# Performance work log

Measured on AMD Instinct MI355X. Metric: run time of the kernel, lower is better.

Reference implementation:

```python
import jax, jax.numpy as jnp
import numpy as np

B, S, H, NH = 8, 1024, 1024, 16
HD = H // NH  # 64


def _rope(x, cos, sin):
    # x: [B, NH, S, HD]; cos/sin: [1, 1, S, HD]
    x1, x2 = jnp.split(x, 2, axis=-1)
    x_rot = jnp.concatenate((-x2, x1), axis=-1)
    return x * cos + x_rot * sin


def setup_inputs() -> dict:
    key = jax.random.key(0)
    ks = jax.random.split(key, 12)
    std = 1.0 / np.sqrt(H)
    inp = {
        "hidden_states": jax.random.normal(ks[0], (B, S, H), dtype=jnp.float32),
        "cos": jax.random.uniform(ks[1], (S, HD), dtype=jnp.float32),
        "sin": jax.random.uniform(ks[2], (S, HD), dtype=jnp.float32),
        "Wq": jax.random.normal(ks[3], (H, H), dtype=jnp.float32) * std,
        "bq": jnp.zeros((H,), dtype=jnp.float32),
        "Wk": jax.random.normal(ks[4], (H, H), dtype=jnp.float32) * std,
        "bk": jnp.zeros((H,), dtype=jnp.float32),
        "Wv": jax.random.normal(ks[5], (H, H), dtype=jnp.float32) * std,
        "bv": jnp.zeros((H,), dtype=jnp.float32),
        "Wo": jax.random.normal(ks[6], (H, H), dtype=jnp.float32) * std,
        "bo": jnp.zeros((H,), dtype=jnp.float32),
    }
    return inp


def reference(hidden_states, cos, sin, Wq, bq, Wk, bk, Wv, bv, Wo, bo):
    def split_heads(t):  # [B,S,H] -> [B,NH,S,HD]
        return t.reshape(B, S, NH, HD).transpose(0, 2, 1, 3)

    q = split_heads(hidden_states @ Wq.T + bq)
    k = split_heads(hidden_states @ Wk.T + bk)
    v = split_heads(hidden_states @ Wv.T + bv)

    c = cos.reshape(1, 1, S, HD)
    s = sin.reshape(1, 1, S, HD)
    q = _rope(q, c, s)
    k = _rope(k, c, s)

    scale = 1.0 / jnp.sqrt(jnp.asarray(HD, dtype=q.dtype))
    scores = jnp.einsum("bhqd,bhkd->bhqk", q, k) * scale
    attn = jax.nn.softmax(scores, axis=-1)
    out = jnp.einsum("bhqk,bhkd->bhqd", attn, v)  # [B,NH,S,HD]
    out = out.transpose(0, 2, 1, 3).reshape(B, S, H)
    return out @ Wo.T + bo
```

## Files before the change

### kernel.cpp

```cpp
#include <hip/hip_runtime.h>
#include <hip/hip_bf16.h>
#include <stdint.h>


typedef __bf16 bf16_t;
typedef __bf16 bf16x8 __attribute__((ext_vector_type(8)));
typedef __bf16 bf16x4 __attribute__((ext_vector_type(4)));
typedef float  f32x4  __attribute__((ext_vector_type(4)));
typedef uint32_t u32x4 __attribute__((ext_vector_type(4)));

typedef __attribute__((address_space(1))) const void* as1_cvp;
typedef __attribute__((address_space(3))) void* as3_vp;

__device__ __forceinline__ f32x4 mfma16(bf16x8 a, bf16x8 b, f32x4 c) {
  return __builtin_amdgcn_mfma_f32_16x16x32_bf16(a, b, c, 0, 0, 0);
}

__device__ __forceinline__ void gload_lds16(const bf16_t* g, bf16_t* l) {
  __builtin_amdgcn_global_load_lds((as1_cvp)g, (as3_vp)l, 16, 0, 0);
}

__device__ __forceinline__ f32x4 zero4() {
  f32x4 z = {0.f, 0.f, 0.f, 0.f};
  return z;
}

__global__ void cvt_all(const float* __restrict__ hs, const float* __restrict__ wq,
                        const float* __restrict__ wk, const float* __restrict__ wv,
                        const float* __restrict__ wo, bf16_t* __restrict__ Xb,
                        bf16_t* __restrict__ Wqkvb, bf16_t* __restrict__ Wob) {
  const int i = blockIdx.x * 256 + threadIdx.x;
  const f32x4* src;
  bf16x4* dst;
  if (i < 2097152) {
    src = (const f32x4*)hs + i;            dst = (bf16x4*)Xb + i;
  } else if (i < 2359296) {
    src = (const f32x4*)wq + (i - 2097152); dst = (bf16x4*)Wqkvb + (i - 2097152);
  } else if (i < 2621440) {
    src = (const f32x4*)wk + (i - 2359296); dst = (bf16x4*)Wqkvb + (i - 2359296) + 262144;
  } else if (i < 2883584) {
    src = (const f32x4*)wv + (i - 2621440); dst = (bf16x4*)Wqkvb + (i - 2621440) + 524288;
  } else {
    src = (const f32x4*)wo + (i - 2883584); dst = (bf16x4*)Wob + (i - 2883584);
  }
  const f32x4 v = *src;
  bf16x4 o;
  o[0] = (bf16_t)v[0]; o[1] = (bf16_t)v[1];
  o[2] = (bf16_t)v[2]; o[3] = (bf16_t)v[3];
  *dst = o;
}

template <int MODE>
__global__ __launch_bounds__(256, 3) void gemm128(
    const bf16_t* __restrict__ A, const bf16_t* __restrict__ Bw,
    const float* __restrict__ bQ, const float* __restrict__ bK,
    const float* __restrict__ bV, const float* __restrict__ cosp,
    const float* __restrict__ sinp,
    bf16_t* __restrict__ Qb, bf16_t* __restrict__ Kb, bf16_t* __restrict__ Vtb,
    float* __restrict__ Cout) {
  __shared__ bf16_t sm[128 * 64 * 2];
  bf16_t* sA = sm;
  bf16_t* sB = sm + 128 * 64;

  const int tid = threadIdx.x;
  const int lane = tid & 63;
  const int wid = tid >> 6;
  const int l15 = lane & 15;
  const int l4 = lane >> 4;
  const int row0 = blockIdx.x * 128;
  const int col0 = blockIdx.y * 128;
  const int wr = (wid >> 1) * 64;
  const int wc = (wid & 1) * 64;

  f32x4 acc[4][4];
#pragma unroll
  for (int mi = 0; mi < 4; ++mi)
#pragma unroll
    for (int ni = 0; ni < 4; ++ni) acc[mi][ni] = zero4();

  for (int kt = 0; kt < 16; ++kt) {
    const int k0 = kt * 64;
#pragma unroll
    for (int i = 0; i < 4; ++i) {
      const int chunk = i * 256 + tid;
      const int r = chunk >> 3, cc = chunk & 7;
      const int scc = cc ^ (r & 7);
      gload_lds16(A + (size_t)(row0 + r) * 1024 + k0 + scc * 8,
                  sA + (i * 256 + wid * 64) * 8);
      gload_lds16(Bw + (size_t)(col0 + r) * 1024 + k0 + scc * 8,
                  sB + (i * 256 + wid * 64) * 8);
    }
    __syncthreads();
    __builtin_amdgcn_s_setprio(1);
#pragma unroll
    for (int ks = 0; ks < 2; ++ks) {
      bf16x8 af[4], bfv[4];
#pragma unroll
      for (int mi = 0; mi < 4; ++mi) {
        const int r = wr + mi * 16 + l15;
        af[mi] = *(const bf16x8*)(sA + r * 64 + (((ks * 4 + l4) ^ (r & 7)) << 3));
      }
#pragma unroll
      for (int ni = 0; ni < 4; ++ni) {
        const int r = wc + ni * 16 + l15;
        bfv[ni] = *(const bf16x8*)(sB + r * 64 + (((ks * 4 + l4) ^ (r & 7)) << 3));
      }
#pragma unroll
      for (int mi = 0; mi < 4; ++mi)
#pragma unroll
        for (int ni = 0; ni < 4; ++ni)
          acc[mi][ni] = mfma16(af[mi], bfv[ni], acc[mi][ni]);
    }
    __builtin_amdgcn_s_setprio(0);
    __syncthreads();
  }

  if constexpr (MODE == 0) {
    const int proj = blockIdx.y >> 3;
    const float* bias = proj == 0 ? bQ : (proj == 1 ? bK : bV);
    if (proj < 2) {
      bf16_t* dst = proj == 0 ? Qb : Kb;
      const float qs = proj == 0 ? 0.18033688011112042f : 1.0f;
      const int base = col0 & 1023;
#pragma unroll
      for (int mi = 0; mi < 4; ++mi)
#pragma unroll
        for (int nl = 0; nl < 2; ++nl) {
          const int gcL = base + wc + nl * 16 + l15;
          const int h = gcL >> 6, dL = gcL & 63;
          const float bbL = bias[gcL], bbH = bias[gcL + 32];
#pragma unroll
          for (int j = 0; j < 4; ++j) {
            const int gr = row0 + wr + mi * 16 + l4 * 4 + j;
            const int b = gr >> 10, s = gr & 1023;
            const float cL = cosp[s * 64 + dL], cH = cosp[s * 64 + dL + 32];
            const float snL = sinp[s * 64 + dL], snH = sinp[s * 64 + dL + 32];
            const float x1 = acc[mi][nl][j] + bbL;
            const float x2 = acc[mi][nl + 2][j] + bbH;
            bf16_t* p = dst + ((size_t)(b * 16 + h) * 1024 + s) * 64 + dL;
            p[0]  = (bf16_t)((x1 * cL - x2 * snL) * qs);
            p[32] = (bf16_t)((x2 * cH + x1 * snH) * qs);
          }
        }
    } else {
      bf16_t* trb = sm;
#pragma unroll
      for (int mi = 0; mi < 4; ++mi)
#pragma unroll
        for (int ni = 0; ni < 4; ++ni) {
          const int cl = wc + ni * 16 + l15;
          const float bb = bias[(col0 & 1023) + cl];
#pragma unroll
          for (int j = 0; j < 4; ++j) {
            const int rl = wr + mi * 16 + l4 * 4 + j;
            trb[cl * 128 + (((rl >> 3) ^ (cl & 7)) << 3) + (rl & 7)] =
                (bf16_t)(acc[mi][ni][j] + bb);
          }
        }
      __syncthreads();
      const int b = row0 >> 10, s0 = row0 & 1023;
#pragma unroll
      for (int i = 0; i < 8; ++i) {
        const int chunk = i * 256 + tid;
        const int cl = chunk >> 4, rc = chunk & 15;
        const u32x4 v = *(const u32x4*)(trb + cl * 128 + ((rc ^ (cl & 7)) << 3));
        const int cv = (col0 & 1023) + cl;
        *(u32x4*)(Vtb + ((size_t)(b * 16 + (cv >> 6)) * 64 + (cv & 63)) * 1024 +
                  s0 + rc * 8) = v;
      }
    }
  } else {
#pragma unroll
    for (int mi = 0; mi < 4; ++mi)
#pragma unroll
      for (int ni = 0; ni < 4; ++ni) {
        const int gc = col0 + wc + ni * 16 + l15;
        const float bb = bQ[gc];
#pragma unroll
        for (int j = 0; j < 4; ++j) {
          const int gr = row0 + wr + mi * 16 + l4 * 4 + j;
          Cout[(size_t)gr * 1024 + gc] = acc[mi][ni][j] + bb;
        }
      }
  }
}

__global__ __launch_bounds__(256, 4) void attn_kernel(
    const bf16_t* __restrict__ Qb, const bf16_t* __restrict__ Kb,
    const bf16_t* __restrict__ Vtb, bf16_t* __restrict__ AOb) {
  __shared__ bf16_t sm[16384];
  bf16_t* sK = sm;
  bf16_t* sV = sm + 4096;
  const int tid = threadIdx.x, lane = tid & 63, wid = tid >> 6;
  const int l15 = lane & 15, l4 = lane >> 4;
  bf16_t* sP = sm + 8192 + wid * 2048;

  const int bh = blockIdx.x;
  const int q0 = blockIdx.y * 128;
  const bf16_t* Qg = Qb + (size_t)bh * 65536;
  const bf16_t* Kg = Kb + (size_t)bh * 65536;
  const bf16_t* Vg = Vtb + (size_t)bh * 65536;

#pragma unroll
  for (int i = 0; i < 4; ++i) {
    const int chunk = i * 256 + tid, r = chunk >> 3, c = chunk & 7;
    *(u32x4*)(sm + r * 64 + ((c ^ (r & 7)) << 3)) =
        *(const u32x4*)(Qg + (size_t)(q0 + r) * 64 + c * 8);
  }
  __syncthreads();
  bf16x8 qf[2][2];
#pragma unroll
  for (int mi = 0; mi < 2; ++mi)
#pragma unroll
    for (int kq = 0; kq < 2; ++kq) {
      const int r = wid * 32 + mi * 16 + l15;
      qf[mi][kq] =
          *(const bf16x8*)(sm + r * 64 + (((kq * 4 + l4) ^ (r & 7)) << 3));
    }
  __syncthreads();

  const int ck0 = tid, ck1 = 256 + tid;
  const int kr0 = ck0 >> 3, kc0 = ck0 & 7;
  const int kr1 = ck1 >> 3, kc1 = ck1 & 7;
  bf16_t* kd0 = sK + kr0 * 64 + ((kc0 ^ (kr0 & 7)) << 3);
  bf16_t* kd1 = sK + kr1 * 64 + ((kc1 ^ (kr1 & 7)) << 3);
  bf16_t* vd0 = sV + kr0 * 64 + ((kc0 ^ (kr0 & 7)) << 3);
  bf16_t* vd1 = sV + kr1 * 64 + ((kc1 ^ (kr1 & 7)) << 3);
  const bf16_t* ksrc0 = Kg + kr0 * 64 + kc0 * 8;
  const bf16_t* ksrc1 = Kg + kr1 * 64 + kc1 * 8;
  const bf16_t* vsrc0 = Vg + kr0 * 1024 + kc0 * 8;
  const bf16_t* vsrc1 = Vg + kr1 * 1024 + kc1 * 8;

  u32x4 kv0 = *(const u32x4*)ksrc0;
  u32x4 kv1 = *(const u32x4*)ksrc1;
  u32x4 kv2 = *(const u32x4*)vsrc0;
  u32x4 kv3 = *(const u32x4*)vsrc1;

  f32x4 oacc[2][4];
  float l_p[2] = {0.f, 0.f};
#pragma unroll
  for (int mi = 0; mi < 2; ++mi)
#pragma unroll
    for (int no = 0; no < 4; ++no) oacc[mi][no] = zero4();

  for (int kt = 0; kt < 16; ++kt) {
    *(u32x4*)kd0 = kv0;
    *(u32x4*)kd1 = kv1;
    *(u32x4*)vd0 = kv2;
    *(u32x4*)vd1 = kv3;
    __syncthreads();
    if (kt < 15) {
      kv0 = *(const u32x4*)(ksrc0 + (kt + 1) * 4096);
      kv1 = *(const u32x4*)(ksrc1 + (kt + 1) * 4096);
      kv2 = *(const u32x4*)(vsrc0 + (kt + 1) * 64);
      kv3 = *(const u32x4*)(vsrc1 + (kt + 1) * 64);
    }

    f32x4 st[2][4];
    __builtin_amdgcn_s_setprio(1);
#pragma unroll
    for (int ni = 0; ni < 4; ++ni) {
      const int r = ni * 16 + l15;
      const bf16x8 kf0 = *(const bf16x8*)(sK + r * 64 + ((l4 ^ (r & 7)) << 3));
      const bf16x8 kf1 =
          *(const bf16x8*)(sK + r * 64 + (((4 + l4) ^ (r & 7)) << 3));
      st[0][ni] = mfma16(kf1, qf[0][1], mfma16(kf0, qf[0][0], zero4()));
      st[1][ni] = mfma16(kf1, qf[1][1], mfma16(kf0, qf[1][0], zero4()));
    }
    __builtin_amdgcn_s_setprio(0);

#pragma unroll
    for (int mi = 0; mi < 2; ++mi) {
      float rs = 0.f;
      const int rl = mi * 16 + l15;
#pragma unroll
      for (int ni = 0; ni < 4; ++ni) {
        bf16x4 pk;
#pragma unroll
        for (int j = 0; j < 4; ++j) {
          const float p = __builtin_amdgcn_exp2f(st[mi][ni][j]);
          rs += p;
          pk[j] = (bf16_t)p;
        }
        const int chunk = (ni * 2 + (l4 >> 1)) ^ (rl & 7);
        *(bf16x4*)(sP + rl * 64 + (chunk << 3) + ((l4 & 1) << 2)) = pk;
      }
      l_p[mi] += rs;
    }

    __builtin_amdgcn_s_setprio(1);
#pragma unroll
    for (int ks = 0; ks < 2; ++ks) {
      bf16x8 pa[2];
#pragma unroll
      for (int mi = 0; mi < 2; ++mi) {
        const int rl = mi * 16 + l15;
        pa[mi] =
            *(const bf16x8*)(sP + rl * 64 + (((ks * 4 + l4) ^ (rl & 7)) << 3));
      }
#pragma unroll
      for (int no = 0; no < 4; ++no) {
        const int hd = no * 16 + l15;
        const bf16x8 vf =
            *(const bf16x8*)(sV + hd * 64 + (((ks * 4 + l4) ^ (hd & 7)) << 3));
        oacc[0][no] = mfma16(pa[0], vf, oacc[0][no]);
        oacc[1][no] = mfma16(pa[1], vf, oacc[1][no]);
      }
    }
    __builtin_amdgcn_s_setprio(0);
    __syncthreads();
  }

  float l_f[2];
#pragma unroll
  for (int mi = 0; mi < 2; ++mi) {
    float t = l_p[mi];
    t += __shfl_xor(t, 16);
    t += __shfl_xor(t, 32);
    l_f[mi] = t;
  }

  const int b = bh >> 4, h = bh & 15;
#pragma unroll
  for (int mi = 0; mi < 2; ++mi)
#pragma unroll
    for (int j = 0; j < 4; ++j) {
      const float li = __builtin_amdgcn_rcpf(__shfl(l_f[mi], l4 * 4 + j));
      const int s = q0 + wid * 32 + mi * 16 + l4 * 4 + j;
#pragma unroll
      for (int no = 0; no < 4; ++no) {
        const int d = no * 16 + l15;
        AOb[((size_t)b * 1024 + s) * 1024 + h * 64 + d] =
            (bf16_t)(oacc[mi][no][j] * li);
      }
    }
}

extern "C" void kernel_launch(void* const* d_in, const int* in_sizes, int n_in,
                              void* d_out, int out_size, void* d_ws,
                              size_t ws_size, hipStream_t stream) {
  const float* hs = (const float*)d_in[0];
  const float* cs = (const float*)d_in[1];
  const float* sn = (const float*)d_in[2];
  const float* Wq = (const float*)d_in[3];
  const float* bq = (const float*)d_in[4];
  const float* Wk = (const float*)d_in[5];
  const float* bk = (const float*)d_in[6];
  const float* Wv = (const float*)d_in[7];
  const float* bv = (const float*)d_in[8];
  const float* Wo = (const float*)d_in[9];
  const float* bo = (const float*)d_in[10];
  float* out = (float*)d_out;

  char* ws = (char*)d_ws;
  bf16_t* Xb    = (bf16_t*)(ws + 0);
  bf16_t* Wqkvb = (bf16_t*)(ws + 16777216);
  bf16_t* Wob   = (bf16_t*)(ws + 23068672);
  bf16_t* Qb    = (bf16_t*)(ws + 25165824);
  bf16_t* Kb    = (bf16_t*)(ws + 41943040);
  bf16_t* Vtb   = (bf16_t*)(ws + 58720256);
  bf16_t* AOb   = (bf16_t*)(ws + 75497472);

  cvt_all<<<12288, 256, 0, stream>>>(hs, Wq, Wk, Wv, Wo, Xb, Wqkvb, Wob);
  gemm128<0><<<dim3(64, 24), 256, 0, stream>>>(Xb, Wqkvb, bq, bk, bv, cs, sn,
                                               Qb, Kb, Vtb, nullptr);
  attn_kernel<<<dim3(128, 8), 256, 0, stream>>>(Qb, Kb, Vtb, AOb);
  gemm128<1><<<dim3(64, 8), 256, 0, stream>>>(AOb, Wob, bo, nullptr, nullptr,
                                              nullptr, nullptr, nullptr,
                                              nullptr, nullptr, out);
}
```

Before: 138.2 us.

## Use 256x256 double-buffered 8-wave GEMM with interleaved prefetch for QKV projection

Replaces the 128x128 QKV projection GEMM with a 256x256-tile, 512-thread kernel. It double-buffers 128 KB of dynamic LDS and issues direct global-to-LDS prefetches of the next K tile between MFMA phases. The split into four sub-phases with barriers and priority bumps is meant to overlap memory traffic with compute and raise data reuse per tile. In exchange the grid drops to 384 blocks, occupancy falls, and the V transpose epilogue now needs two passes.

```diff
diff --git a/kernel.cpp b/kernel.cpp
--- a/kernel.cpp
+++ b/kernel.cpp
@@ -50,18 +50,200 @@
   *dst = o;
 }
 
-template <int MODE>
-__global__ __launch_bounds__(256, 3) void gemm128(
+__global__ __launch_bounds__(512, 2) void gemm256_qkv(
     const bf16_t* __restrict__ A, const bf16_t* __restrict__ Bw,
     const float* __restrict__ bQ, const float* __restrict__ bK,
     const float* __restrict__ bV, const float* __restrict__ cosp,
     const float* __restrict__ sinp,
-    bf16_t* __restrict__ Qb, bf16_t* __restrict__ Kb, bf16_t* __restrict__ Vtb,
-    float* __restrict__ Cout) {
+    bf16_t* __restrict__ Qb, bf16_t* __restrict__ Kb, bf16_t* __restrict__ Vtb) {
+  extern __shared__ bf16_t smem[];
+  const int tid = threadIdx.x;
+  const int lane = tid & 63, wid = tid >> 6;
+  const int l15 = lane & 15, l4 = lane >> 4;
+  const int wr = wid >> 2, wc = wid & 3;
+  const int row0 = blockIdx.x * 256, col0 = blockIdx.y * 256;
+
+  const int rr = tid >> 3, cc8 = tid & 7;
+  const int sc = cc8 ^ (rr & 7);
+  const bf16_t* pAs = A + (size_t)(row0 + rr) * 1024 + sc * 8;
+  const bf16_t* pBs = Bw + (size_t)(col0 + rr) * 1024 + sc * 8;
+  const int dA = wid * 512;
+
+  f32x4 acc[8][4];
+#pragma unroll
+  for (int mi = 0; mi < 8; ++mi)
+#pragma unroll
+    for (int ni = 0; ni < 4; ++ni) acc[mi][ni] = zero4();
+
+#pragma unroll
+  for (int k = 0; k < 4; ++k)
+    gload_lds16(pAs + (size_t)k * 65536, smem + k * 4096 + dA);
+#pragma unroll
+  for (int k = 0; k < 4; ++k)
+    gload_lds16(pBs + (size_t)k * 65536, smem + 16384 + k * 4096 + dA);
+  asm volatile("s_waitcnt vmcnt(0)" ::: "memory");
+  __builtin_amdgcn_s_barrier();
+
+#pragma unroll 2
+  for (int t = 0; t < 16; ++t) {
+    const int cur = t & 1;
+    bf16_t* sA = smem + cur * 32768;
+    bf16_t* sB = sA + 16384;
+    bf16_t* oD = smem + (cur ^ 1) * 32768;
+    const size_t ko = (size_t)(t + 1) * 64;
+
+    bf16x8 a0[4][2], a1[4][2], b0[2][2], b1[2][2];
+#pragma unroll
+    for (int mi = 0; mi < 4; ++mi) {
+      const int r = wr * 128 + mi * 16 + l15;
+#pragma unroll
+      for (int ks = 0; ks < 2; ++ks)
+        a0[mi][ks] = *(const bf16x8*)(sA + r * 64 + (((ks * 4 + l4) ^ (r & 7)) << 3));
+    }
+#pragma unroll
+    for (int n = 0; n < 2; ++n) {
+      const int r = wc * 64 + n * 16 + l15;
+#pragma unroll
+      for (int ks = 0; ks < 2; ++ks)
+        b0[n][ks] = *(const bf16x8*)(sB + r * 64 + (((ks * 4 + l4) ^ (r & 7)) << 3));
+    }
+    if (t < 15) {
+#pragma unroll
+      for (int k = 0; k < 4; ++k)
+        gload_lds16(pAs + (size_t)k * 65536 + ko, oD + k * 4096 + dA);
+    }
+    __builtin_amdgcn_s_barrier();
+    __builtin_amdgcn_s_setprio(1);
+#pragma unroll
+    for (int mi = 0; mi < 4; ++mi)
+#pragma unroll
+      for (int n = 0; n < 2; ++n)
+        acc[mi][n] = mfma16(a0[mi][1], b0[n][1],
+                            mfma16(a0[mi][0], b0[n][0], acc[mi][n]));
+    __builtin_amdgcn_s_setprio(0);
+    __builtin_amdgcn_s_barrier();
+
+#pragma unroll
+    for (int mi = 0; mi < 4; ++mi) {
+      const int r = wr * 128 + (mi + 4) * 16 + l15;
+#pragma unroll
+      for (int ks = 0; ks < 2; ++ks)
+        a1[mi][ks] = *(const bf16x8*)(sA + r * 64 + (((ks * 4 + l4) ^ (r & 7)) << 3));
+    }
+    if (t < 15) {
+#pragma unroll
+      for (int k = 0; k < 4; ++k)
+        gload_lds16(pBs + (size_t)k * 65536 + ko, oD + 16384 + k * 4096 + dA);
+    }
+    __builtin_amdgcn_s_barrier();
+    __builtin_amdgcn_s_setprio(1);
+#pragma unroll
+    for (int mi = 0; mi < 4; ++mi)
+#pragma unroll
+      for (int n = 0; n < 2; ++n)
+        acc[mi + 4][n] = mfma16(a1[mi][1], b0[n][1],
+                                mfma16(a1[mi][0], b0[n][0], acc[mi + 4][n]));
+    __builtin_amdgcn_s_setprio(0);
+    __builtin_amdgcn_s_barrier();
+
+#pragma unroll
+    for (int n = 0; n < 2; ++n) {
+      const int r = wc * 64 + (n + 2) * 16 + l15;
+#pragma unroll
+      for (int ks = 0; ks < 2; ++ks)
+        b1[n][ks] = *(const bf16x8*)(sB + r * 64 + (((ks * 4 + l4) ^ (r & 7)) << 3));
+    }
+    __builtin_amdgcn_s_barrier();
+    __builtin_amdgcn_s_setprio(1);
+#pragma unroll
+    for (int mi = 0; mi < 4; ++mi)
+#pragma unroll
+      for (int n = 0; n < 2; ++n)
+        acc[mi][n + 2] = mfma16(a0[mi][1], b1[n][1],
+                                mfma16(a0[mi][0], b1[n][0], acc[mi][n + 2]));
+    __builtin_amdgcn_s_setprio(0);
+    __builtin_amdgcn_s_barrier();
+
+    __builtin_amdgcn_s_setprio(1);
+#pragma unroll
+    for (int mi = 0; mi < 4; ++mi)
+#pragma unroll
+      for (int n = 0; n < 2; ++n)
+        acc[mi + 4][n + 2] = mfma16(a1[mi][1], b1[n][1],
+                                    mfma16(a1[mi][0], b1[n][0], acc[mi + 4][n + 2]));
+    __builtin_amdgcn_s_setprio(0);
+    if (t < 15) asm volatile("s_waitcnt vmcnt(0)" ::: "memory");
+    __builtin_amdgcn_s_barrier();
+  }
+
+  const int proj = col0 >> 10;
+  const int colp = col0 & 1023;
+  if (proj < 2) {
+    const float* bias = proj == 0 ? bQ : bK;
+    bf16_t* dst = proj == 0 ? Qb : Kb;
+    const float qs = proj == 0 ? 0.18033688011112042f : 1.0f;
+#pragma unroll
+    for (int mi = 0; mi < 8; ++mi)
+#pragma unroll
+      for (int nl = 0; nl < 2; ++nl) {
+        const int gcL = colp + wc * 64 + nl * 16 + l15;
+        const int h = gcL >> 6, dL = gcL & 63;
+        const float bbL = bias[gcL], bbH = bias[gcL + 32];
+#pragma unroll
+        for (int j = 0; j < 4; ++j) {
+          const int gr = row0 + wr * 128 + mi * 16 + l4 * 4 + j;
+          const int b = gr >> 10, s = gr & 1023;
+          const float cL = cosp[s * 64 + dL], cH = cosp[s * 64 + dL + 32];
+          const float snL = sinp[s * 64 + dL], snH = sinp[s * 64 + dL + 32];
+          const float x1 = acc[mi][nl][j] + bbL;
+          const float x2 = acc[mi][nl + 2][j] + bbH;
+          bf16_t* p = dst + ((size_t)(b * 16 + h) * 1024 + s) * 64 + dL;
+          p[0]  = (bf16_t)((x1 * cL - x2 * snL) * qs);
+          p[32] = (bf16_t)((x2 * cH + x1 * snH) * qs);
+        }
+      }
+  } else {
+    const int b = row0 >> 10, s0 = row0 & 1023;
+    __syncthreads();
+    bf16_t* trb = smem;
+#pragma unroll
+    for (int pass = 0; pass < 2; ++pass) {
+      if (wr == pass) {
+#pragma unroll
+        for (int mi = 0; mi < 8; ++mi)
+#pragma unroll
+          for (int ni = 0; ni < 4; ++ni) {
+            const int cl = wc * 64 + ni * 16 + l15;
+            const float bb = bV[colp + cl];
+#pragma unroll
+            for (int j = 0; j < 4; ++j) {
+              const int rl = mi * 16 + l4 * 4 + j;
+              trb[cl * 128 + (((rl >> 3) ^ (cl & 7)) << 3) + (rl & 7)] =
+                  (bf16_t)(acc[mi][ni][j] + bb);
+            }
+          }
+      }
+      __syncthreads();
+#pragma unroll
+      for (int i = 0; i < 8; ++i) {
+        const int chunk = i * 512 + tid;
+        const int cl = chunk >> 4, rc = chunk & 15;
+        const u32x4 v = *(const u32x4*)(trb + cl * 128 + ((rc ^ (cl & 7)) << 3));
+        const int cv = colp + cl;
+        *(u32x4*)(Vtb + ((size_t)(b * 16 + (cv >> 6)) * 64 + (cv & 63)) * 1024 +
+                  s0 + pass * 128 + rc * 8) = v;
+      }
+      __syncthreads();
+    }
+  }
+}
+
+__global__ __launch_bounds__(256, 3) void gemm128_out(
+    const bf16_t* __restrict__ A, const bf16_t* __restrict__ Bw,
+    const float* __restrict__ bo, float* __restrict__ Cout) {
   __shared__ bf16_t sm[128 * 64 * 2];
   bf16_t* sA = sm;
   bf16_t* sB = sm + 128 * 64;
-
   const int tid = threadIdx.x;
   const int lane = tid & 63;
   const int wid = tid >> 6;
@@ -115,74 +297,18 @@
     __syncthreads();
   }
 
-  if constexpr (MODE == 0) {
-    const int proj = blockIdx.y >> 3;
-    const float* bias = proj == 0 ? bQ : (proj == 1 ? bK : bV);
-    if (proj < 2) {
-      bf16_t* dst = proj == 0 ? Qb : Kb;
-      const float qs = proj == 0 ? 0.18033688011112042f : 1.0f;
-      const int base = col0 & 1023;
-#pragma unroll
-      for (int mi = 0; mi < 4; ++mi)
-#pragma unroll
-        for (int nl = 0; nl < 2; ++nl) {
-          const int gcL = base + wc + nl * 16 + l15;
-          const int h = gcL >> 6, dL = gcL & 63;
-          const float bbL = bias[gcL], bbH = bias[gcL + 32];
-#pragma unroll
-          for (int j = 0; j < 4; ++j) {
-            const int gr = row0 + wr + mi * 16 + l4 * 4 + j;
-            const int b = gr >> 10, s = gr & 1023;
-            const float cL = cosp[s * 64 + dL], cH = cosp[s * 64 + dL + 32];
-            const float snL = sinp[s * 64 + dL], snH = sinp[s * 64 + dL + 32];
-            const float x1 = acc[mi][nl][j] + bbL;
-            const float x2 = acc[mi][nl + 2][j] + bbH;
-            bf16_t* p = dst + ((size_t)(b * 16 + h) * 1024 + s) * 64 + dL;
-            p[0]  = (bf16_t)((x1 * cL - x2 * snL) * qs);
-            p[32] = (bf16_t)((x2 * cH + x1 * snH) * qs);
-          }
-        }
-    } else {
-      bf16_t* trb = sm;
-#pragma unroll
-      for (int mi = 0; mi < 4; ++mi)
-#pragma unroll
-        for (int ni = 0; ni < 4; ++ni) {
-          const int cl = wc + ni * 16 + l15;
-          const float bb = bias[(col0 & 1023) + cl];
-#pragma unroll
-          for (int j = 0; j < 4; ++j) {
-            const int rl = wr + mi * 16 + l4 * 4 + j;
-            trb[cl * 128 + (((rl >> 3) ^ (cl & 7)) << 3) + (rl & 7)] =
-                (bf16_t)(acc[mi][ni][j] + bb);
-          }
-        }
-      __syncthreads();
-      const int b = row0 >> 10, s0 = row0 & 1023;
-#pragma unroll
-      for (int i = 0; i < 8; ++i) {
-        const int chunk = i * 256 + tid;
-        const int cl = chunk >> 4, rc = chunk & 15;
-        const u32x4 v = *(const u32x4*)(trb + cl * 128 + ((rc ^ (cl & 7)) << 3));
-        const int cv = (col0 & 1023) + cl;
-        *(u32x4*)(Vtb + ((size_t)(b * 16 + (cv >> 6)) * 64 + (cv & 63)) * 1024 +
-                  s0 + rc * 8) = v;
-      }
-    }
-  } else {
-#pragma unroll
-    for (int mi = 0; mi < 4; ++mi)
-#pragma unroll
-      for (int ni = 0; ni < 4; ++ni) {
-        const int gc = col0 + wc + ni * 16 + l15;
-        const float bb = bQ[gc];
-#pragma unroll
-        for (int j = 0; j < 4; ++j) {
-          const int gr = row0 + wr + mi * 16 + l4 * 4 + j;
-          Cout[(size_t)gr * 1024 + gc] = acc[mi][ni][j] + bb;
-        }
-      }
-  }
+#pragma unroll
+  for (int mi = 0; mi < 4; ++mi)
+#pragma unroll
+    for (int ni = 0; ni < 4; ++ni) {
+      const int gc = col0 + wc + ni * 16 + l15;
+      const float bb = bo[gc];
+#pragma unroll
+      for (int j = 0; j < 4; ++j) {
+        const int gr = row0 + wr + mi * 16 + l4 * 4 + j;
+        Cout[(size_t)gr * 1024 + gc] = acc[mi][ni][j] + bb;
+      }
+    }
 }
 
 __global__ __launch_bounds__(256, 4) void attn_kernel(
@@ -219,8 +345,8 @@
     }
   __syncthreads();
 
-  const int ck0 = tid, ck1 = 256 + tid;
-  const int kr0 = ck0 >> 3, kc0 = ck0 & 7;
+  const int ck1 = 256 + tid;
+  const int kr0 = tid >> 3, kc0 = tid & 7;
   const int kr1 = ck1 >> 3, kc1 = ck1 & 7;
   bf16_t* kd0 = sK + kr0 * 64 + ((kc0 ^ (kr0 & 7)) << 3);
   bf16_t* kd1 = sK + kr1 * 64 + ((kc1 ^ (kr1 & 7)) << 3);
@@ -361,11 +487,12 @@
   bf16_t* Vtb   = (bf16_t*)(ws + 58720256);
   bf16_t* AOb   = (bf16_t*)(ws + 75497472);
 
+  (void)hipFuncSetAttribute((const void*)gemm256_qkv,
+                            hipFuncAttributeMaxDynamicSharedMemorySize, 131072);
+
   cvt_all<<<12288, 256, 0, stream>>>(hs, Wq, Wk, Wv, Wo, Xb, Wqkvb, Wob);
-  gemm128<0><<<dim3(64, 24), 256, 0, stream>>>(Xb, Wqkvb, bq, bk, bv, cs, sn,
-                                               Qb, Kb, Vtb, nullptr);
+  gemm256_qkv<<<dim3(32, 12), 512, 131072, stream>>>(Xb, Wqkvb, bq, bk, bv, cs,
+                                                     sn, Qb, Kb, Vtb);
   attn_kernel<<<dim3(128, 8), 256, 0, stream>>>(Qb, Kb, Vtb, AOb);
-  gemm128<1><<<dim3(64, 8), 256, 0, stream>>>(AOb, Wob, bo, nullptr, nullptr,
-                                              nullptr, nullptr, nullptr,
-                                              nullptr, nullptr, out);
-}
+  gemm128_out<<<dim3(64, 8), 256, 0, stream>>>(AOb, Wob, bo, out);
+}
```

After: 147.4 us. 6.7% more time.

## Rewrite attention with 32x32 MFMA, register-resident P, and 256-query tiles

Applied to the files above, without the earlier changes.

The attention kernel moves from 16x16x32 to 32x32x16 bf16 MFMA tiles. Each block now covers 256 queries, with 64 per wave, so K/V tiles are reused across twice as many queries and the grid is halved. The softmax probabilities are no longer staged through LDS: they are packed to bf16 and exchanged between half-waves with a cross-lane shuffle so they can feed the PV MFMA directly as the operand layout. Launch bounds drop to 2 blocks per SM to allow more registers, which lowers occupancy, and the 512-block grid may leave some CUs idle.

```diff
diff --git a/kernel.cpp b/kernel.cpp
--- a/kernel.cpp
+++ b/kernel.cpp
@@ -7,6 +7,7 @@
 typedef __bf16 bf16x8 __attribute__((ext_vector_type(8)));
 typedef __bf16 bf16x4 __attribute__((ext_vector_type(4)));
 typedef float  f32x4  __attribute__((ext_vector_type(4)));
+typedef float  f32x16 __attribute__((ext_vector_type(16)));
 typedef uint32_t u32x4 __attribute__((ext_vector_type(4)));
 
 typedef __attribute__((address_space(1))) const void* as1_cvp;
@@ -14,6 +15,9 @@
 
 __device__ __forceinline__ f32x4 mfma16(bf16x8 a, bf16x8 b, f32x4 c) {
   return __builtin_amdgcn_mfma_f32_16x16x32_bf16(a, b, c, 0, 0, 0);
+}
+__device__ __forceinline__ f32x16 mfma32(bf16x8 a, bf16x8 b, f32x16 c) {
+  return __builtin_amdgcn_mfma_f32_32x32x16_bf16(a, b, c, 0, 0, 0);
 }
 
 __device__ __forceinline__ void gload_lds16(const bf16_t* g, bf16_t* l) {
@@ -23,6 +27,13 @@
 __device__ __forceinline__ f32x4 zero4() {
   f32x4 z = {0.f, 0.f, 0.f, 0.f};
   return z;
+}
+
+__device__ __forceinline__ uint32_t pk2(float a, float b) {
+  union { bf16_t h[2]; uint32_t u; } x;
+  x.h[0] = (bf16_t)a;
+  x.h[1] = (bf16_t)b;
+  return x.u;
 }
 
 __global__ void cvt_all(const float* __restrict__ hs, const float* __restrict__ wq,
@@ -185,42 +196,42 @@
   }
 }
 
-__global__ __launch_bounds__(256, 4) void attn_kernel(
+__global__ __launch_bounds__(256, 2) void attn_kernel(
     const bf16_t* __restrict__ Qb, const bf16_t* __restrict__ Kb,
     const bf16_t* __restrict__ Vtb, bf16_t* __restrict__ AOb) {
   __shared__ bf16_t sm[16384];
   bf16_t* sK = sm;
   bf16_t* sV = sm + 4096;
   const int tid = threadIdx.x, lane = tid & 63, wid = tid >> 6;
-  const int l15 = lane & 15, l4 = lane >> 4;
-  bf16_t* sP = sm + 8192 + wid * 2048;
+  const int l31 = lane & 31, l5 = lane >> 5;
+  const bool loh = (l5 == 0);
 
   const int bh = blockIdx.x;
-  const int q0 = blockIdx.y * 128;
+  const int q0 = blockIdx.y * 256;
   const bf16_t* Qg = Qb + (size_t)bh * 65536;
   const bf16_t* Kg = Kb + (size_t)bh * 65536;
   const bf16_t* Vg = Vtb + (size_t)bh * 65536;
 
 #pragma unroll
-  for (int i = 0; i < 4; ++i) {
+  for (int i = 0; i < 8; ++i) {
     const int chunk = i * 256 + tid, r = chunk >> 3, c = chunk & 7;
     *(u32x4*)(sm + r * 64 + ((c ^ (r & 7)) << 3)) =
         *(const u32x4*)(Qg + (size_t)(q0 + r) * 64 + c * 8);
   }
   __syncthreads();
-  bf16x8 qf[2][2];
-#pragma unroll
-  for (int mi = 0; mi < 2; ++mi)
-#pragma unroll
-    for (int kq = 0; kq < 2; ++kq) {
-      const int r = wid * 32 + mi * 16 + l15;
-      qf[mi][kq] =
-          *(const bf16x8*)(sm + r * 64 + (((kq * 4 + l4) ^ (r & 7)) << 3));
+  bf16x8 qf[2][4];
+#pragma unroll
+  for (int qb = 0; qb < 2; ++qb)
+#pragma unroll
+    for (int step = 0; step < 4; ++step) {
+      const int r = wid * 64 + qb * 32 + l31;
+      qf[qb][step] =
+          *(const bf16x8*)(sm + r * 64 + (((step * 2 + l5) ^ (r & 7)) << 3));
     }
   __syncthreads();
 
-  const int ck0 = tid, ck1 = 256 + tid;
-  const int kr0 = ck0 >> 3, kc0 = ck0 & 7;
+  const int ck1 = 256 + tid;
+  const int kr0 = tid >> 3, kc0 = tid & 7;
   const int kr1 = ck1 >> 3, kc1 = ck1 & 7;
   bf16_t* kd0 = sK + kr0 * 64 + ((kc0 ^ (kr0 & 7)) << 3);
   bf16_t* kd1 = sK + kr1 * 64 + ((kc1 ^ (kr1 & 7)) << 3);
@@ -236,12 +247,14 @@
   u32x4 kv2 = *(const u32x4*)vsrc0;
   u32x4 kv3 = *(const u32x4*)vsrc1;
 
-  f32x4 oacc[2][4];
+  f32x16 accO[2][2];
+#pragma unroll
+  for (int qb = 0; qb < 2; ++qb)
+#pragma unroll
+    for (int db = 0; db < 2; ++db)
+#pragma unroll
+      for (int r = 0; r < 16; ++r) accO[qb][db][r] = 0.f;
   float l_p[2] = {0.f, 0.f};
-#pragma unroll
-  for (int mi = 0; mi < 2; ++mi)
-#pragma unroll
-    for (int no = 0; no < 4; ++no) oacc[mi][no] = zero4();
 
   for (int kt = 0; kt < 16; ++kt) {
     *(u32x4*)kd0 = kv0;
@@ -256,84 +269,108 @@
       kv3 = *(const u32x4*)(vsrc1 + (kt + 1) * 64);
     }
 
-    f32x4 st[2][4];
-    __builtin_amdgcn_s_setprio(1);
-#pragma unroll
-    for (int ni = 0; ni < 4; ++ni) {
-      const int r = ni * 16 + l15;
-      const bf16x8 kf0 = *(const bf16x8*)(sK + r * 64 + ((l4 ^ (r & 7)) << 3));
-      const bf16x8 kf1 =
-          *(const bf16x8*)(sK + r * 64 + (((4 + l4) ^ (r & 7)) << 3));
-      st[0][ni] = mfma16(kf1, qf[0][1], mfma16(kf0, qf[0][0], zero4()));
-      st[1][ni] = mfma16(kf1, qf[1][1], mfma16(kf0, qf[1][0], zero4()));
-    }
-    __builtin_amdgcn_s_setprio(0);
-
-#pragma unroll
-    for (int mi = 0; mi < 2; ++mi) {
-      float rs = 0.f;
-      const int rl = mi * 16 + l15;
-#pragma unroll
-      for (int ni = 0; ni < 4; ++ni) {
-        bf16x4 pk;
-#pragma unroll
-        for (int j = 0; j < 4; ++j) {
-          const float p = __builtin_amdgcn_exp2f(st[mi][ni][j]);
-          rs += p;
-          pk[j] = (bf16_t)p;
+#pragma unroll
+    for (int kb = 0; kb < 2; ++kb) {
+      bf16x8 kf[4];
+#pragma unroll
+      for (int step = 0; step < 4; ++step) {
+        const int r = kb * 32 + l31;
+        kf[step] =
+            *(const bf16x8*)(sK + r * 64 + (((step * 2 + l5) ^ (r & 7)) << 3));
+      }
+      f32x16 st0, st1;
+#pragma unroll
+      for (int r = 0; r < 16; ++r) { st0[r] = 0.f; st1[r] = 0.f; }
+      __builtin_amdgcn_s_setprio(1);
+#pragma unroll
+      for (int step = 0; step < 4; ++step)
+        st0 = mfma32(kf[step], qf[0][step], st0);
+#pragma unroll
+      for (int step = 0; step < 4; ++step)
+        st1 = mfma32(kf[step], qf[1][step], st1);
+      __builtin_amdgcn_s_setprio(0);
+
+      float p0[16], p1[16];
+      float rs0 = 0.f, rs1 = 0.f;
+#pragma unroll
+      for (int r = 0; r < 16; ++r) {
+        p0[r] = __builtin_amdgcn_exp2f(st0[r]);
+        rs0 += p0[r];
+        p1[r] = __builtin_amdgcn_exp2f(st1[r]);
+        rs1 += p1[r];
+      }
+      l_p[0] += rs0;
+      l_p[1] += rs1;
+
+#pragma unroll
+      for (int cb = 0; cb < 2; ++cb) {
+        const int c = kb * 2 + cb;
+        const uint32_t A0q0 = pk2(p0[8 * cb + 0], p0[8 * cb + 1]);
+        const uint32_t B0q0 = pk2(p0[8 * cb + 2], p0[8 * cb + 3]);
+        const uint32_t A1q0 = pk2(p0[8 * cb + 4], p0[8 * cb + 5]);
+        const uint32_t B1q0 = pk2(p0[8 * cb + 6], p0[8 * cb + 7]);
+        const uint32_t TAq0 = __shfl_xor(loh ? A1q0 : A0q0, 32);
+        const uint32_t TBq0 = __shfl_xor(loh ? B1q0 : B0q0, 32);
+        u32x4 w0;
+        w0[0] = loh ? A0q0 : TAq0;
+        w0[1] = loh ? B0q0 : TBq0;
+        w0[2] = loh ? TAq0 : A1q0;
+        w0[3] = loh ? TBq0 : B1q0;
+        const bf16x8 pa0 = __builtin_bit_cast(bf16x8, w0);
+        const uint32_t A0q1 = pk2(p1[8 * cb + 0], p1[8 * cb + 1]);
+        const uint32_t B0q1 = pk2(p1[8 * cb + 2], p1[8 * cb + 3]);
+        const uint32_t A1q1 = pk2(p1[8 * cb + 4], p1[8 * cb + 5]);
+        const uint32_t B1q1 = pk2(p1[8 * cb + 6], p1[8 * cb + 7]);
+        const uint32_t TAq1 = __shfl_xor(loh ? A1q1 : A0q1, 32);
+        const uint32_t TBq1 = __shfl_xor(loh ? B1q1 : B0q1, 32);
+        u32x4 w1;
+        w1[0] = loh ? A0q1 : TAq1;
+        w1[1] = loh ? B0q1 : TBq1;
+        w1[2] = loh ? TAq1 : A1q1;
+        w1[3] = loh ? TBq1 : B1q1;
+        const bf16x8 pa1 = __builtin_bit_cast(bf16x8, w1);
+
+        bf16x8 vf[2];
+#pragma unroll
+        for (int db = 0; db < 2; ++db) {
+          const int d = db * 32 + l31;
+          vf[db] =
+              *(const bf16x8*)(sV + d * 64 + (((c * 2 + l5) ^ (d & 7)) << 3));
         }
-        const int chunk = (ni * 2 + (l4 >> 1)) ^ (rl & 7);
-        *(bf16x4*)(sP + rl * 64 + (chunk << 3) + ((l4 & 1) << 2)) = pk;
-      }
-      l_p[mi] += rs;
-    }
-
-    __builtin_amdgcn_s_setprio(1);
-#pragma unroll
-    for (int ks = 0; ks < 2; ++ks) {
-      bf16x8 pa[2];
-#pragma unroll
-      for (int mi = 0; mi < 2; ++mi) {
-        const int rl = mi * 16 + l15;
-        pa[mi] =
-            *(const bf16x8*)(sP + rl * 64 + (((ks * 4 + l4) ^ (rl & 7)) << 3));
-      }
-#pragma unroll
-      for (int no = 0; no < 4; ++no) {
-        const int hd = no * 16 + l15;
-        const bf16x8 vf =
-            *(const bf16x8*)(sV + hd * 64 + (((ks * 4 + l4) ^ (hd & 7)) << 3));
-        oacc[0][no] = mfma16(pa[0], vf, oacc[0][no]);
-        oacc[1][no] = mfma16(pa[1], vf, oacc[1][no]);
-      }
-    }
-    __builtin_amdgcn_s_setprio(0);
+        __builtin_amdgcn_s_setprio(1);
+        accO[0][0] = mfma32(vf[0], pa0, accO[0][0]);
+        accO[0][1] = mfma32(vf[1], pa0, accO[0][1]);
+        accO[1][0] = mfma32(vf[0], pa1, accO[1][0]);
+        accO[1][1] = mfma32(vf[1], pa1, accO[1][1]);
+        __builtin_amdgcn_s_setprio(0);
+      }
+    }
     __syncthreads();
   }
 
-  float l_f[2];
-#pragma unroll
-  for (int mi = 0; mi < 2; ++mi) {
-    float t = l_p[mi];
-    t += __shfl_xor(t, 16);
-    t += __shfl_xor(t, 32);
-    l_f[mi] = t;
+  float li[2];
+#pragma unroll
+  for (int qb = 0; qb < 2; ++qb) {
+    const float t = l_p[qb] + __shfl_xor(l_p[qb], 32);
+    li[qb] = __builtin_amdgcn_rcpf(t);
   }
 
   const int b = bh >> 4, h = bh & 15;
 #pragma unroll
-  for (int mi = 0; mi < 2; ++mi)
-#pragma unroll
-    for (int j = 0; j < 4; ++j) {
-      const float li = __builtin_amdgcn_rcpf(__shfl(l_f[mi], l4 * 4 + j));
-      const int s = q0 + wid * 32 + mi * 16 + l4 * 4 + j;
-#pragma unroll
-      for (int no = 0; no < 4; ++no) {
-        const int d = no * 16 + l15;
-        AOb[((size_t)b * 1024 + s) * 1024 + h * 64 + d] =
-            (bf16_t)(oacc[mi][no][j] * li);
-      }
-    }
+  for (int qb = 0; qb < 2; ++qb) {
+    const int s = q0 + wid * 64 + qb * 32 + l31;
+    bf16_t* rowp = AOb + ((size_t)b * 1024 + s) * 1024 + h * 64;
+#pragma unroll
+    for (int db = 0; db < 2; ++db)
+#pragma unroll
+      for (int g = 0; g < 4; ++g) {
+        bf16x4 o;
+#pragma unroll
+        for (int j = 0; j < 4; ++j)
+          o[j] = (bf16_t)(accO[qb][db][g * 4 + j] * li[qb]);
+        *(bf16x4*)(rowp + db * 32 + g * 8 + l5 * 4) = o;
+      }
+  }
 }
 
 extern "C" void kernel_launch(void* const* d_in, const int* in_sizes, int n_in,
@@ -364,7 +401,7 @@
   cvt_all<<<12288, 256, 0, stream>>>(hs, Wq, Wk, Wv, Wo, Xb, Wqkvb, Wob);
   gemm128<0><<<dim3(64, 24), 256, 0, stream>>>(Xb, Wqkvb, bq, bk, bv, cs, sn,
                                                Qb, Kb, Vtb, nullptr);
-  attn_kernel<<<dim3(128, 8), 256, 0, stream>>>(Qb, Kb, Vtb, AOb);
+  attn_kernel<<<dim3(128, 4), 256, 0, stream>>>(Qb, Kb, Vtb, AOb);
   gemm128<1><<<dim3(64, 8), 256, 0, stream>>>(AOb, Wob, bo, nullptr, nullptr,
                                               nullptr, nullptr, nullptr,
                                               nullptr, nullptr, out);
```

After: 138.4 us. No clear change (+0.1%).
